# Performance work log

Hardware: AMD Instinct MI355X
Metric: run time of the kernel (lower is better)

The kernel has to match this reference:

```python
import jax, jax.numpy as jnp
import numpy as np

B, S, QD, KVD, H = 8, 1024, 1024, 1024, 8
NEG_SLOPE = 0.01


def _lin(t, w, b):
    # torch nn.Linear: y = x @ W^T + b, W is (out, in)
    return t @ w.T + b


def _heads(t, n_head):
    b, s, e = t.shape
    return t.reshape(b, s, n_head, e // n_head).transpose(0, 2, 1, 3)  # (B,H,S,D)


def _merge(t):
    b, h, s, d = t.shape
    return t.transpose(0, 2, 1, 3).reshape(b, s, h * d)


def setup_inputs() -> dict:
    key = jax.random.key(0)
    ks = iter(jax.random.split(key, 64))

    def W(shape):
        return (jax.random.normal(next(ks), shape, jnp.float32) * 0.02)

    inp = {
        'x': jax.random.normal(next(ks), (B, S, QD), jnp.float32),
        'y': jax.random.normal(next(ks), (B, S, KVD), jnp.float32),
        # cross-attention projections
        'ca_q_w': W((QD, QD)), 'ca_q_b': W((QD,)),
        'ca_qv_w': W((QD, QD)), 'ca_qv_b': W((QD,)),
        'ca_k_w': W((QD, KVD)), 'ca_k_b': W((QD,)),
        'ca_kv_w': W((QD, KVD)), 'ca_kv_b': W((QD,)),
        'ca_o_w': W((QD, QD)), 'ca_o_b': W((QD,)),
        # LayerNorm over [seq_len, q_dim]
        'ln_w': jnp.ones((S, QD), jnp.float32),
        'ln_b': jnp.zeros((S, QD), jnp.float32),
        # 3-layer FeedForward
        'ff1_w': W((QD, QD)), 'ff1_b': W((QD,)),
        'ff2_w': W((QD, QD)), 'ff2_b': W((QD,)),
        'ff3_w': W((QD, QD)), 'ff3_b': W((QD,)),
        # self-attention 1
        'sa1_q_w': W((QD, QD)), 'sa1_q_b': W((QD,)),
        'sa1_k_w': W((QD, QD)), 'sa1_k_b': W((QD,)),
        'sa1_v_w': W((QD, QD)), 'sa1_v_b': W((QD,)),
        'sa1_o_w': W((QD, QD)), 'sa1_o_b': W((QD,)),
        # self-attention 2
        'sa2_q_w': W((QD, QD)), 'sa2_q_b': W((QD,)),
        'sa2_k_w': W((QD, QD)), 'sa2_k_b': W((QD,)),
        'sa2_v_w': W((QD, QD)), 'sa2_v_b': W((QD,)),
        'sa2_o_w': W((QD, QD)), 'sa2_o_b': W((QD,)),
    }
    return inp


def _self_attn(t, qw, qb, kw, kb, vw, vb, ow, ob):
    q = _heads(_lin(t, qw, qb), H)
    k = _heads(_lin(t, kw, kb), H)
    v = _heads(_lin(t, vw, vb), H)
    scale = 1.0 / jnp.sqrt(jnp.asarray(q.shape[-1], q.dtype))
    a = jax.nn.softmax(jnp.einsum('bhsd,bhtd->bhst', q, k) * scale, axis=-1)
    return _lin(_merge(jnp.einsum('bhst,bhtd->bhsd', a, v)), ow, ob)


def reference(x, y, ca_q_w, ca_q_b, ca_qv_w, ca_qv_b, ca_k_w, ca_k_b, ca_kv_w, ca_kv_b, ca_o_w, ca_o_b, ln_w, ln_b, ff1_w, ff1_b, ff2_w, ff2_b, ff3_w, ff3_b, sa1_q_w, sa1_q_b, sa1_k_w, sa1_k_b, sa1_v_w, sa1_v_b, sa1_o_w, sa1_o_b, sa2_q_w, sa2_q_b, sa2_k_w, sa2_k_b, sa2_v_w, sa2_v_b, sa2_o_w, sa2_o_b):
    # --- FlowFace cross-attention (no 1/sqrt(d) scaling, +QV term) ---
    q = _heads(_lin(x, ca_q_w, ca_q_b), H)
    qv = _heads(_lin(x, ca_qv_w, ca_qv_b), H)
    k = _heads(_lin(y, ca_k_w, ca_k_b), H)
    kv = _heads(_lin(y, ca_kv_w, ca_kv_b), H)
    attn = jax.nn.softmax(jnp.einsum('bhsd,bhtd->bhst', q, k), axis=-1)
    ca = _lin(_merge(jnp.einsum('bhst,bhtd->bhsd', attn, kv) + qv), ca_o_w, ca_o_b)
    h1 = x + ca
    # --- LayerNorm over last two dims [seq_len, q_dim] ---
    mu = h1.mean(axis=(-2, -1), keepdims=True)
    var = h1.var(axis=(-2, -1), keepdims=True)
    hn = (h1 - mu) / jnp.sqrt(var + 1e-5) * ln_w + ln_b
    # --- 3-layer FeedForward with leaky_relu + residual ---
    lr = lambda t: jax.nn.leaky_relu(t, NEG_SLOPE)
    f = lr(_lin(lr(_lin(lr(_lin(hn, ff1_w, ff1_b)), ff2_w, ff2_b)), ff3_w, ff3_b))
    h2 = hn + f
    # --- two self-attention layers ---
    h3 = _self_attn(h2, sa1_q_w, sa1_q_b, sa1_k_w, sa1_k_b, sa1_v_w, sa1_v_b, sa1_o_w, sa1_o_b)
    out = _self_attn(h3, sa2_q_w, sa2_q_b, sa2_k_w, sa2_k_b, sa2_v_w, sa2_v_b, sa2_o_w, sa2_o_b)
    return out
```

## Files before the change

kernel.cpp:

```cpp
#include <hip/hip_runtime.h>
#include <cstdint>
#include <cstddef>

#define DI __device__ __forceinline__

typedef __bf16 bf16x8 __attribute__((ext_vector_type(8)));
typedef float  f32x4  __attribute__((ext_vector_type(4)));

constexpr int kE = 1024;
constexpr int kM = 8192;
constexpr float kSlope = 0.01f;

DI float bf2f(ushort u) { union { uint32_t i; float f; } v; v.i = ((uint32_t)u) << 16; return v.f; }
DI ushort f2bf(float f) {
    union { float f; uint32_t i; } v; v.f = f;
    return (ushort)((v.i + 0x7FFFu + ((v.i >> 16) & 1u)) >> 16);
}
DI bf16x8 ld8f(const float* p) {
    const float4 f0 = *(const float4*)p;
    const float4 f1 = *(const float4*)(p + 4);
    union { bf16x8 v; ushort u[8]; } o;
    o.u[0] = f2bf(f0.x); o.u[1] = f2bf(f0.y); o.u[2] = f2bf(f0.z); o.u[3] = f2bf(f0.w);
    o.u[4] = f2bf(f1.x); o.u[5] = f2bf(f1.y); o.u[6] = f2bf(f1.z); o.u[7] = f2bf(f1.w);
    return o.v;
}
template<typename T> DI float ldf(const T* p);
template<> DI float ldf<ushort>(const ushort* p) { return bf2f(*p); }
template<> DI float ldf<float>(const float* p) { return *p; }

DI void gload16(const void* g, void* lds) {
    __builtin_amdgcn_global_load_lds((const __attribute__((address_space(1))) void*)g,
                                     (__attribute__((address_space(3))) void*)lds, 16, 0, 0);
}

DI int swz7(int r) { return ((r ^ (r >> 3)) & 7) << 4; }

struct PtrTab { const float* w[16]; const float* b[16]; const float* x; const float* y; };

__global__ __launch_bounds__(256)
void cvt_pack(PtrTab t, ushort* __restrict__ WB, ushort* __restrict__ Xb,
              ushort* __restrict__ Yb, float* __restrict__ BP)
{
    const int blk = blockIdx.x, tid = threadIdx.x;
    if (blk < 16384) {
        const float* src; ushort* dst; size_t idx;
        if (blk < 8192)       { const int w = blk >> 9; idx = (size_t)(blk & 511) * 2048 + tid * 8; src = t.w[w]; dst = WB + (size_t)w * 1048576; }
        else if (blk < 12288) { idx = (size_t)(blk - 8192) * 2048 + tid * 8;  src = t.x; dst = Xb; }
        else                  { idx = (size_t)(blk - 12288) * 2048 + tid * 8; src = t.y; dst = Yb; }
        *(bf16x8*)(dst + idx) = ld8f(src + idx);
    } else {
        const size_t i = (size_t)(blk - 16384) * 2048 + tid * 8;
        const int w = (int)(i >> 10), off = (int)(i & 1023);
        *(float4*)(BP + i)     = *(const float4*)(t.b[w] + off);
        *(float4*)(BP + i + 4) = *(const float4*)(t.b[w] + off + 4);
    }
}

template<int ACT, int RESID, int VT, typename TR, typename TO>
__global__ __launch_bounds__(256)
void gemm_bf16(const ushort* __restrict__ A, const ushort* __restrict__ W,
               const float* __restrict__ bias, const TR* __restrict__ resb,
               TO* __restrict__ out, int N, ushort* __restrict__ vt_out, int vtcol0)
{
    __shared__ __align__(16) char sm[2][16384];
    constexpr int K = 1024;
    const int tid = threadIdx.x, l = tid & 63, wid = tid >> 6;
    const int wm = wid >> 1, wn = wid & 1;

    const int cpx = gridDim.x >> 3;
    const int sb = (blockIdx.x & 7) * cpx + (blockIdx.x >> 3);
    const int nbn = N >> 7;
    const int bm = sb / nbn, bn = sb - bm * nbn;
    const size_t row0 = (size_t)bm << 7, col0 = (size_t)bn << 7;
    const bool isvt = VT && ((int)col0 >= vtcol0);

    const int o0 = (wid * 2) * 1024 + (l << 4), o1 = o0 + 1024;
    const int r0s = o0 >> 6, c0s = ((o0 >> 4) & 3) ^ ((r0s >> 1) & 3);
    const int r1s = o1 >> 6, c1s = ((o1 >> 4) & 3) ^ ((r1s >> 1) & 3);
    const ushort* gA0 = A + (row0 + r0s) * K + c0s * 8;
    const ushort* gA1 = A + (row0 + r1s) * K + c1s * 8;
    const ushort* gW0 = W + (col0 + r0s) * K + c0s * 8;
    const ushort* gW1 = W + (col0 + r1s) * K + c1s * 8;
    const int d0 = (wid * 2) * 1024, d1 = d0 + 1024;

    f32x4 acc[4][4] = {};

    {
        gload16(gA0, sm[0] + d0); gload16(gA1, sm[0] + d1);
        gload16(gW0, sm[0] + 8192 + d0); gload16(gW1, sm[0] + 8192 + d1);
    }
    __syncthreads();

    for (int kt = 0; kt < 32; ++kt) {
        const int cur = kt & 1;
        if (kt + 1 < 32) {
            const int ko = (kt + 1) << 5;
            char* nb = sm[cur ^ 1];
            gload16(gA0 + ko, nb + d0); gload16(gA1 + ko, nb + d1);
            gload16(gW0 + ko, nb + 8192 + d0); gload16(gW1 + ko, nb + 8192 + d1);
        }
        const char* At = sm[cur];
        const char* Wt = sm[cur] + 8192;
        bf16x8 af[4], bfr[4];
        #pragma unroll
        for (int mi = 0; mi < 4; ++mi) {
            const int r = (wm << 6) + (mi << 4) + (l & 15);
            af[mi] = *(const bf16x8*)(At + r * 64 + ((((l >> 4) ^ ((r >> 1) & 3))) << 4));
        }
        #pragma unroll
        for (int ni = 0; ni < 4; ++ni) {
            const int r = (wn << 6) + (ni << 4) + (l & 15);
            bfr[ni] = *(const bf16x8*)(Wt + r * 64 + ((((l >> 4) ^ ((r >> 1) & 3))) << 4));
        }
        if (!isvt) {
            #pragma unroll
            for (int mi = 0; mi < 4; ++mi)
                #pragma unroll
                for (int ni = 0; ni < 4; ++ni)
                    acc[mi][ni] = __builtin_amdgcn_mfma_f32_16x16x32_bf16(af[mi], bfr[ni], acc[mi][ni], 0, 0, 0);
        } else {
            #pragma unroll
            for (int mi = 0; mi < 4; ++mi)
                #pragma unroll
                for (int ni = 0; ni < 4; ++ni)
                    acc[mi][ni] = __builtin_amdgcn_mfma_f32_16x16x32_bf16(bfr[ni], af[mi], acc[mi][ni], 0, 0, 0);
        }
        __syncthreads();
    }

    const int cr = (l >> 4) << 2, cc = l & 15;
    if (!isvt) {
        #pragma unroll
        for (int mi = 0; mi < 4; ++mi) {
            #pragma unroll
            for (int ni = 0; ni < 4; ++ni) {
                const size_t gr = row0 + (wm << 6) + (mi << 4) + cr;
                const size_t gc = col0 + (wn << 6) + (ni << 4) + cc;
                const float bv = bias[gc];
                #pragma unroll
                for (int r = 0; r < 4; ++r) {
                    float v = acc[mi][ni][r] + bv;
                    if (ACT) v = v > 0.f ? v : v * kSlope;
                    const size_t off = (gr + r) * (size_t)N + gc;
                    if (RESID) v += ldf(resb + off);
                    if constexpr (sizeof(TO) == 4) out[off] = v;
                    else                           out[off] = f2bf(v);
                }
            }
        }
    } else if (VT) {
        #pragma unroll
        for (int mi = 0; mi < 4; ++mi) {
            const size_t t_glob = row0 + (wm << 6) + (mi << 4) + cc;
            const size_t bb = t_glob >> 10;
            const int tt = (int)(t_glob & 1023);
            #pragma unroll
            for (int ni = 0; ni < 4; ++ni) {
                const int gcb = (int)col0 + (wn << 6) + (ni << 4) + cr;
                const int dbase = gcb - vtcol0;
                #pragma unroll
                for (int r = 0; r < 4; ++r) {
                    const float v = acc[mi][ni][r] + bias[gcb + r];
                    vt_out[(((bb << 10) + dbase + r) << 10) + tt] = f2bf(v);
                }
            }
        }
    }
}

template<int ADD_QV>
__global__ __launch_bounds__(256)
void attn_fwd(const ushort* __restrict__ Q, const ushort* __restrict__ K,
              const ushort* __restrict__ VT, const ushort* __restrict__ QV,
              ushort* __restrict__ O, int ld, float scale)
{
    __shared__ __align__(16) char Kt[64 * 256];
    __shared__ __align__(16) char Vt[128 * 128];
    __shared__ __align__(16) char Pl[4][2048];

    const int tid = threadIdx.x;
    const int l = tid & 63, w = tid >> 6;

    const int cpx = gridDim.x >> 3;
    const int sb = (blockIdx.x & 7) * cpx + (blockIdx.x >> 3);
    const int qt = sb & 15;
    const int bh = sb >> 4;
    const int h = bh & 7, b = bh >> 3;

    const size_t bi = ((size_t)b << 10) * (size_t)ld + ((size_t)h << 7);
    const size_t bo = ((size_t)b << 10) * 1024 + ((size_t)h << 7);
    const size_t vtoff = ((size_t)bh) << 17;
    const size_t qrow0 = (size_t)(qt << 6) + (w << 4);

    bf16x8 qf[4];
    #pragma unroll
    for (int kk = 0; kk < 4; ++kk)
        qf[kk] = *(const bf16x8*)(Q + bi + (qrow0 + (l & 15)) * ld + (kk << 5) + ((l >> 4) << 3));

    f32x4 oacc[8] = {};
    float mrow[4] = {-1e30f, -1e30f, -1e30f, -1e30f};
    float lrow[4] = {0.f, 0.f, 0.f, 0.f};

    const int sr = tid >> 4, sc = tid & 15;

    int vofs[4];
    #pragma unroll
    for (int it = 0; it < 4; ++it) {
        const int d = it * 32 + (tid >> 3);
        const int s = tid & 7;
        const int c = s ^ ((d ^ (d >> 3)) & 7);
        vofs[it] = d * 1024 + c * 8;
    }
    const int vdst = tid * 16;

    for (int kt0 = 0; kt0 < 16; ++kt0) {
        __syncthreads();
        #pragma unroll
        for (int it = 0; it < 4; ++it) {
            const int r = sr + (it << 4);
            uint4 kv = *(const uint4*)(K + bi + (size_t)(kt0 * 64 + r) * ld + (sc << 3));
            *(uint4*)(Kt + r * 256 + ((sc << 4) ^ swz7(r))) = kv;
        }
        #pragma unroll
        for (int it = 0; it < 4; ++it) {
            uint4 vv = *(const uint4*)(VT + vtoff + (size_t)(kt0 << 6) + vofs[it]);
            *(uint4*)(Vt + it * 4096 + vdst) = vv;
        }
        __syncthreads();

        f32x4 sacc[4] = {};
        #pragma unroll
        for (int ni = 0; ni < 4; ++ni) {
            const int r = (l & 15) + (ni << 4);
            #pragma unroll
            for (int kk = 0; kk < 4; ++kk) {
                bf16x8 kf = *(const bf16x8*)(Kt + r * 256 + ((((kk << 2) + (l >> 4)) << 4) ^ swz7(r)));
                sacc[ni] = __builtin_amdgcn_mfma_f32_16x16x32_bf16(qf[kk], kf, sacc[ni], 0, 0, 0);
            }
        }
        #pragma unroll
        for (int ni = 0; ni < 4; ++ni) sacc[ni] *= scale;

        float corr[4];
        #pragma unroll
        for (int r = 0; r < 4; ++r) {
            float m0 = fmaxf(fmaxf(sacc[0][r], sacc[1][r]), fmaxf(sacc[2][r], sacc[3][r]));
            #pragma unroll
            for (int m = 1; m < 16; m <<= 1) m0 = fmaxf(m0, __shfl_xor(m0, m, 64));
            const float mn = fmaxf(mrow[r], m0);
            corr[r] = __expf(mrow[r] - mn);
            mrow[r] = mn;
        }
        float ps[4] = {0.f, 0.f, 0.f, 0.f};
        ushort pb[4][4];
        #pragma unroll
        for (int ni = 0; ni < 4; ++ni)
            #pragma unroll
            for (int r = 0; r < 4; ++r) {
                const float p = __expf(sacc[ni][r] - mrow[r]);
                ps[r] += p;
                pb[ni][r] = f2bf(p);
            }
        #pragma unroll
        for (int r = 0; r < 4; ++r) {
            float s = ps[r];
            #pragma unroll
            for (int m = 1; m < 16; m <<= 1) s += __shfl_xor(s, m, 64);
            lrow[r] = lrow[r] * corr[r] + s;
        }
        #pragma unroll
        for (int nd = 0; nd < 8; ++nd)
            #pragma unroll
            for (int r = 0; r < 4; ++r) oacc[nd][r] *= corr[r];

        char* pw = Pl[w];
        #pragma unroll
        for (int ni = 0; ni < 4; ++ni)
            #pragma unroll
            for (int r = 0; r < 4; ++r) {
                const int q = ((l >> 4) << 2) + r;
                const int t = (l & 15) + (ni << 4);
                *(ushort*)(pw + q * 128 + ((t * 2) ^ swz7(q))) = pb[ni][r];
            }
        #pragma unroll
        for (int tg = 0; tg < 2; ++tg) {
            const int q = l & 15;
            bf16x8 pf = *(const bf16x8*)(pw + q * 128 + ((((tg << 2) + (l >> 4)) << 4) ^ swz7(q)));
            #pragma unroll
            for (int nd = 0; nd < 8; ++nd) {
                const int d = (nd << 4) + (l & 15);
                const int m = (d ^ (d >> 3)) & 7;
                bf16x8 vf = *(const bf16x8*)(Vt + d * 128 + ((((tg << 2) + (l >> 4)) ^ m) << 4));
                oacc[nd] = __builtin_amdgcn_mfma_f32_16x16x32_bf16(pf, vf, oacc[nd], 0, 0, 0);
            }
        }
    }

    const size_t orow = qrow0 + ((l >> 4) << 2);
    #pragma unroll
    for (int r = 0; r < 4; ++r) {
        const float inv = 1.f / lrow[r];
        #pragma unroll
        for (int nd = 0; nd < 8; ++nd) {
            const size_t c = (l & 15) + (nd << 4);
            float v = oacc[nd][r] * inv;
            if (ADD_QV) v += bf2f(QV[bi + (orow + r) * ld + c]);
            O[bo + (orow + r) * 1024 + c] = f2bf(v);
        }
    }
}

__global__ void ln_partial(const ushort* __restrict__ h1, float2* __restrict__ part)
{
    __shared__ float sa[8];
    const size_t off = ((size_t)blockIdx.x) << 15;
    float s = 0.f, s2 = 0.f;
    for (int i = threadIdx.x; i < 4096; i += 256) {
        uint4 u = *(const uint4*)(h1 + off + (size_t)i * 8);
        const ushort* e = (const ushort*)&u;
        #pragma unroll
        for (int j = 0; j < 8; ++j) { const float v = bf2f(e[j]); s += v; s2 += v * v; }
    }
    #pragma unroll
    for (int m = 1; m < 64; m <<= 1) { s += __shfl_xor(s, m, 64); s2 += __shfl_xor(s2, m, 64); }
    const int w = threadIdx.x >> 6;
    if ((threadIdx.x & 63) == 0) { sa[w * 2] = s; sa[w * 2 + 1] = s2; }
    __syncthreads();
    if (threadIdx.x == 0)
        part[blockIdx.x] = make_float2(sa[0] + sa[2] + sa[4] + sa[6], sa[1] + sa[3] + sa[5] + sa[7]);
}

__global__ void ln_finish(const float2* __restrict__ part, float2* __restrict__ stats)
{
    const int b = threadIdx.x;
    if (b < 8) {
        float s = 0.f, s2 = 0.f;
        for (int c = 0; c < 32; ++c) { const float2 v = part[b * 32 + c]; s += v.x; s2 += v.y; }
        const float mu = s * (1.f / 1048576.f);
        const float var = s2 * (1.f / 1048576.f) - mu * mu;
        stats[b] = make_float2(mu, rsqrtf(var + 1e-5f));
    }
}

__global__ void ln_apply(const ushort* __restrict__ h1, const float2* __restrict__ stats,
                         const float* __restrict__ gw, const float* __restrict__ gb,
                         ushort* __restrict__ hn)
{
    const size_t i = ((size_t)blockIdx.x * 256 + threadIdx.x) * 8;
    const int b = (int)(i >> 20);
    const size_t r = i & 1048575;
    const float2 st = stats[b];
    uint4 uv = *(const uint4*)(h1 + i);
    const float4 w0 = *(const float4*)(gw + r);
    const float4 w1 = *(const float4*)(gw + r + 4);
    const float4 b0 = *(const float4*)(gb + r);
    const float4 b1 = *(const float4*)(gb + r + 4);
    const float wv[8] = {w0.x, w0.y, w0.z, w0.w, w1.x, w1.y, w1.z, w1.w};
    const float bv[8] = {b0.x, b0.y, b0.z, b0.w, b1.x, b1.y, b1.z, b1.w};
    const ushort* ev = (const ushort*)&uv;
    ushort o[8];
    #pragma unroll
    for (int j = 0; j < 8; ++j)
        o[j] = f2bf((bf2f(ev[j]) - st.x) * st.y * wv[j] + bv[j]);
    *(uint4*)(hn + i) = *(const uint4*)o;
}

extern "C" void kernel_launch(void* const* d_in, const int* in_sizes, int n_in,
                              void* d_out, int out_size, void* d_ws, size_t ws_size,
                              hipStream_t stream)
{
    (void)in_sizes; (void)n_in; (void)out_size; (void)ws_size;
    auto P = [&](int i) { return (const float*)d_in[i]; };

    const size_t MB = 1u << 20;
    char* ws = (char*)d_ws;
    ushort* WB = (ushort*)ws;
    ushort* R0 = (ushort*)(ws + 32 * MB);
    ushort* R1 = (ushort*)(ws + 64 * MB);
    ushort* A0 = (ushort*)(ws + 96 * MB);
    ushort* A1 = (ushort*)(ws + 112 * MB);
    float*  BP = (float*)(ws + 128 * MB);
    float2* PART = (float2*)(ws + 128 * MB + 65536);
    float2* STATS = PART + 256;

    PtrTab tab;
    const int wsrc[16] = {2,4,6,8,10,14,16,18,20,22,24,26,28,30,32,34};
    for (int i = 0; i < 16; ++i) { tab.w[i] = P(wsrc[i]); tab.b[i] = P(wsrc[i] + 1); }
    tab.x = P(0); tab.y = P(1);

    const dim3 blk(256);
    const float SA_SCALE = 0.08838834764831845f;
    auto Wp = [&](int w) { return WB + (size_t)w * 1048576; };
    auto Bp = [&](int w) { return BP + (size_t)w * 1024; };

    cvt_pack<<<dim3(16392), blk, 0, stream>>>(tab, WB, A0, A1, BP);

    gemm_bf16<0,0,0,ushort,ushort><<<dim3(1024), blk, 0, stream>>>(A0, Wp(0), Bp(0), (const ushort*)nullptr, R0, 2048, nullptr, 0);
    gemm_bf16<0,0,1,ushort,ushort><<<dim3(1024), blk, 0, stream>>>(A1, Wp(2), Bp(2), (const ushort*)nullptr, R1, 2048, A0, 1024);
    attn_fwd<1><<<dim3(1024), blk, 0, stream>>>(R0, R1, A0, R0 + 1024, A1, 2048, 1.0f);
    gemm_bf16<0,1,0,float,ushort><<<dim3(512), blk, 0, stream>>>(A1, Wp(4), Bp(4), P(0), A0, 1024, nullptr, 0);

    ln_partial<<<dim3(256), blk, 0, stream>>>(A0, PART);
    ln_finish<<<dim3(1), dim3(64), 0, stream>>>(PART, STATS);
    ln_apply<<<dim3(4096), blk, 0, stream>>>(A0, STATS, P(12), P(13), A1);

    gemm_bf16<1,0,0,ushort,ushort><<<dim3(512), blk, 0, stream>>>(A1, Wp(5), Bp(5), (const ushort*)nullptr, R0, 1024, nullptr, 0);
    gemm_bf16<1,0,0,ushort,ushort><<<dim3(512), blk, 0, stream>>>(R0, Wp(6), Bp(6), (const ushort*)nullptr, R1, 1024, nullptr, 0);
    gemm_bf16<1,1,0,ushort,ushort><<<dim3(512), blk, 0, stream>>>(R1, Wp(7), Bp(7), A1, A0, 1024, nullptr, 0);

    gemm_bf16<0,0,1,ushort,ushort><<<dim3(1536), blk, 0, stream>>>(A0, Wp(8), Bp(8), (const ushort*)nullptr, R0, 3072, A1, 2048);
    attn_fwd<0><<<dim3(1024), blk, 0, stream>>>(R0, R0 + 1024, A1, nullptr, A0, 3072, SA_SCALE);
    gemm_bf16<0,0,0,ushort,ushort><<<dim3(512), blk, 0, stream>>>(A0, Wp(11), Bp(11), (const ushort*)nullptr, A1, 1024, nullptr, 0);

    gemm_bf16<0,0,1,ushort,ushort><<<dim3(1536), blk, 0, stream>>>(A1, Wp(12), Bp(12), (const ushort*)nullptr, R0, 3072, A0, 2048);
    attn_fwd<0><<<dim3(1024), blk, 0, stream>>>(R0, R0 + 1024, A0, nullptr, A1, 3072, SA_SCALE);
    gemm_bf16<0,0,0,ushort,float><<<dim3(512), blk, 0, stream>>>(A1, Wp(15), Bp(15), (const ushort*)nullptr, (float*)d_out, 1024, nullptr, 0);
}
```

Baseline: 876.3 us.

## Add 256x256-tile GEMM kernel for wide fused QKV projections

Adds a new 512-thread GEMM kernel with 256x256 output tiles and 8x4 MFMA accumulators per wave, and uses it for the wide fused projection GEMMs (N=2048/3072), including the transposed-V write path. The 128x128 kernel is kept for the N=1024 GEMMs but loses its VT path. Larger tiles raise arithmetic intensity and cut redundant A/W loads. The cost is more registers and LDS per block and fewer blocks (256/384) to spread across the CUs, which can leave wave slots idle.

```diff
diff --git a/kernel.cpp b/kernel.cpp
--- a/kernel.cpp
+++ b/kernel.cpp
@@ -56,11 +56,11 @@
     }
 }
 
-template<int ACT, int RESID, int VT, typename TR, typename TO>
+template<int ACT, int RESID, typename TR, typename TO>
 __global__ __launch_bounds__(256)
 void gemm_bf16(const ushort* __restrict__ A, const ushort* __restrict__ W,
                const float* __restrict__ bias, const TR* __restrict__ resb,
-               TO* __restrict__ out, int N, ushort* __restrict__ vt_out, int vtcol0)
+               TO* __restrict__ out, int N)
 {
     __shared__ __align__(16) char sm[2][16384];
     constexpr int K = 1024;
@@ -72,7 +72,6 @@
     const int nbn = N >> 7;
     const int bm = sb / nbn, bn = sb - bm * nbn;
     const size_t row0 = (size_t)bm << 7, col0 = (size_t)bn << 7;
-    const bool isvt = VT && ((int)col0 >= vtcol0);
 
     const int o0 = (wid * 2) * 1024 + (l << 4), o1 = o0 + 1024;
     const int r0s = o0 >> 6, c0s = ((o0 >> 4) & 3) ^ ((r0s >> 1) & 3);
@@ -112,15 +111,96 @@
             const int r = (wn << 6) + (ni << 4) + (l & 15);
             bfr[ni] = *(const bf16x8*)(Wt + r * 64 + ((((l >> 4) ^ ((r >> 1) & 3))) << 4));
         }
+        #pragma unroll
+        for (int mi = 0; mi < 4; ++mi)
+            #pragma unroll
+            for (int ni = 0; ni < 4; ++ni)
+                acc[mi][ni] = __builtin_amdgcn_mfma_f32_16x16x32_bf16(af[mi], bfr[ni], acc[mi][ni], 0, 0, 0);
+        __syncthreads();
+    }
+
+    const int cr = (l >> 4) << 2, cc = l & 15;
+    #pragma unroll
+    for (int mi = 0; mi < 4; ++mi) {
+        #pragma unroll
+        for (int ni = 0; ni < 4; ++ni) {
+            const size_t gr = row0 + (wm << 6) + (mi << 4) + cr;
+            const size_t gc = col0 + (wn << 6) + (ni << 4) + cc;
+            const float bv = bias[gc];
+            #pragma unroll
+            for (int r = 0; r < 4; ++r) {
+                float v = acc[mi][ni][r] + bv;
+                if (ACT) v = v > 0.f ? v : v * kSlope;
+                const size_t off = (gr + r) * (size_t)N + gc;
+                if (RESID) v += ldf(resb + off);
+                if constexpr (sizeof(TO) == 4) out[off] = v;
+                else                           out[off] = f2bf(v);
+            }
+        }
+    }
+}
+
+template<int VT>
+__global__ __launch_bounds__(512, 2)
+void gemm256(const ushort* __restrict__ A, const ushort* __restrict__ W,
+             const float* __restrict__ bias, ushort* __restrict__ out, int N,
+             ushort* __restrict__ vt_out, int vtcol0)
+{
+    __shared__ __align__(16) char sm[2][32768];
+    constexpr int K = 1024;
+    const int tid = threadIdx.x, l = tid & 63, wid = tid >> 6;
+    const int wm = wid >> 2, wn = wid & 3;
+
+    const int cpx = gridDim.x >> 3;
+    const int sb = (blockIdx.x & 7) * cpx + (blockIdx.x >> 3);
+    const int nbn = N >> 8;
+    const int bm = sb / nbn, bn = sb - bm * nbn;
+    const size_t row0 = (size_t)bm << 8, col0 = (size_t)bn << 8;
+    const bool isvt = VT && ((int)col0 >= vtcol0);
+
+    const int r0s = tid >> 2, c0s = (tid & 3) ^ ((r0s >> 1) & 3);
+    const ushort* gA0 = A + (row0 + r0s) * K + c0s * 8;
+    const ushort* gA1 = gA0 + (size_t)128 * K;
+    const ushort* gW0 = W + (col0 + r0s) * K + c0s * 8;
+    const ushort* gW1 = gW0 + (size_t)128 * K;
+    const int d0 = wid * 1024;
+
+    f32x4 acc[8][4] = {};
+
+    gload16(gA0, sm[0] + d0);          gload16(gA1, sm[0] + 8192 + d0);
+    gload16(gW0, sm[0] + 16384 + d0);  gload16(gW1, sm[0] + 24576 + d0);
+    __syncthreads();
+
+    for (int kt = 0; kt < 32; ++kt) {
+        const int cur = kt & 1;
+        if (kt + 1 < 32) {
+            const int ko = (kt + 1) << 5;
+            char* nb = sm[cur ^ 1];
+            gload16(gA0 + ko, nb + d0);          gload16(gA1 + ko, nb + 8192 + d0);
+            gload16(gW0 + ko, nb + 16384 + d0);  gload16(gW1 + ko, nb + 24576 + d0);
+        }
+        const char* At = sm[cur];
+        const char* Wt = sm[cur] + 16384;
+        bf16x8 af[8], bfr[4];
+        #pragma unroll
+        for (int mi = 0; mi < 8; ++mi) {
+            const int r = (wm << 7) + (mi << 4) + (l & 15);
+            af[mi] = *(const bf16x8*)(At + r * 64 + (((l >> 4) ^ ((r >> 1) & 3)) << 4));
+        }
+        #pragma unroll
+        for (int ni = 0; ni < 4; ++ni) {
+            const int r = (wn << 6) + (ni << 4) + (l & 15);
+            bfr[ni] = *(const bf16x8*)(Wt + r * 64 + (((l >> 4) ^ ((r >> 1) & 3)) << 4));
+        }
         if (!isvt) {
             #pragma unroll
-            for (int mi = 0; mi < 4; ++mi)
+            for (int mi = 0; mi < 8; ++mi)
                 #pragma unroll
                 for (int ni = 0; ni < 4; ++ni)
                     acc[mi][ni] = __builtin_amdgcn_mfma_f32_16x16x32_bf16(af[mi], bfr[ni], acc[mi][ni], 0, 0, 0);
         } else {
             #pragma unroll
-            for (int mi = 0; mi < 4; ++mi)
+            for (int mi = 0; mi < 8; ++mi)
                 #pragma unroll
                 for (int ni = 0; ni < 4; ++ni)
                     acc[mi][ni] = __builtin_amdgcn_mfma_f32_16x16x32_bf16(bfr[ni], af[mi], acc[mi][ni], 0, 0, 0);
@@ -131,27 +211,23 @@
     const int cr = (l >> 4) << 2, cc = l & 15;
     if (!isvt) {
         #pragma unroll
-        for (int mi = 0; mi < 4; ++mi) {
+        for (int mi = 0; mi < 8; ++mi) {
             #pragma unroll
             for (int ni = 0; ni < 4; ++ni) {
-                const size_t gr = row0 + (wm << 6) + (mi << 4) + cr;
+                const size_t gr = row0 + (wm << 7) + (mi << 4) + cr;
                 const size_t gc = col0 + (wn << 6) + (ni << 4) + cc;
                 const float bv = bias[gc];
                 #pragma unroll
                 for (int r = 0; r < 4; ++r) {
-                    float v = acc[mi][ni][r] + bv;
-                    if (ACT) v = v > 0.f ? v : v * kSlope;
-                    const size_t off = (gr + r) * (size_t)N + gc;
-                    if (RESID) v += ldf(resb + off);
-                    if constexpr (sizeof(TO) == 4) out[off] = v;
-                    else                           out[off] = f2bf(v);
+                    const float v = acc[mi][ni][r] + bv;
+                    out[(gr + r) * (size_t)N + gc] = f2bf(v);
                 }
             }
         }
     } else if (VT) {
         #pragma unroll
-        for (int mi = 0; mi < 4; ++mi) {
-            const size_t t_glob = row0 + (wm << 6) + (mi << 4) + cc;
+        for (int mi = 0; mi < 8; ++mi) {
+            const size_t t_glob = row0 + (wm << 7) + (mi << 4) + cc;
             const size_t bb = t_glob >> 10;
             const int tt = (int)(t_glob & 1023);
             #pragma unroll
@@ -388,31 +464,31 @@
     for (int i = 0; i < 16; ++i) { tab.w[i] = P(wsrc[i]); tab.b[i] = P(wsrc[i] + 1); }
     tab.x = P(0); tab.y = P(1);
 
-    const dim3 blk(256);
+    const dim3 blk(256), blk5(512);
     const float SA_SCALE = 0.08838834764831845f;
     auto Wp = [&](int w) { return WB + (size_t)w * 1048576; };
     auto Bp = [&](int w) { return BP + (size_t)w * 1024; };
 
     cvt_pack<<<dim3(16392), blk, 0, stream>>>(tab, WB, A0, A1, BP);
 
-    gemm_bf16<0,0,0,ushort,ushort><<<dim3(1024), blk, 0, stream>>>(A0, Wp(0), Bp(0), (const ushort*)nullptr, R0, 2048, nullptr, 0);
-    gemm_bf16<0,0,1,ushort,ushort><<<dim3(1024), blk, 0, stream>>>(A1, Wp(2), Bp(2), (const ushort*)nullptr, R1, 2048, A0, 1024);
+    gemm256<0><<<dim3(256), blk5, 0, stream>>>(A0, Wp(0), Bp(0), R0, 2048, nullptr, 0);
+    gemm256<1><<<dim3(256), blk5, 0, stream>>>(A1, Wp(2), Bp(2), R1, 2048, A0, 1024);
     attn_fwd<1><<<dim3(1024), blk, 0, stream>>>(R0, R1, A0, R0 + 1024, A1, 2048, 1.0f);
-    gemm_bf16<0,1,0,float,ushort><<<dim3(512), blk, 0, stream>>>(A1, Wp(4), Bp(4), P(0), A0, 1024, nullptr, 0);
+    gemm_bf16<0,1,float,ushort><<<dim3(512), blk, 0, stream>>>(A1, Wp(4), Bp(4), P(0), A0, 1024);
 
     ln_partial<<<dim3(256), blk, 0, stream>>>(A0, PART);
     ln_finish<<<dim3(1), dim3(64), 0, stream>>>(PART, STATS);
     ln_apply<<<dim3(4096), blk, 0, stream>>>(A0, STATS, P(12), P(13), A1);
 
-    gemm_bf16<1,0,0,ushort,ushort><<<dim3(512), blk, 0, stream>>>(A1, Wp(5), Bp(5), (const ushort*)nullptr, R0, 1024, nullptr, 0);
-    gemm_bf16<1,0,0,ushort,ushort><<<dim3(512), blk, 0, stream>>>(R0, Wp(6), Bp(6), (const ushort*)nullptr, R1, 1024, nullptr, 0);
-    gemm_bf16<1,1,0,ushort,ushort><<<dim3(512), blk, 0, stream>>>(R1, Wp(7), Bp(7), A1, A0, 1024, nullptr, 0);
-
-    gemm_bf16<0,0,1,ushort,ushort><<<dim3(1536), blk, 0, stream>>>(A0, Wp(8), Bp(8), (const ushort*)nullptr, R0, 3072, A1, 2048);
+    gemm_bf16<1,0,ushort,ushort><<<dim3(512), blk, 0, stream>>>(A1, Wp(5), Bp(5), (const ushort*)nullptr, R0, 1024);
+    gemm_bf16<1,0,ushort,ushort><<<dim3(512), blk, 0, stream>>>(R0, Wp(6), Bp(6), (const ushort*)nullptr, R1, 1024);
+    gemm_bf16<1,1,ushort,ushort><<<dim3(512), blk, 0, stream>>>(R1, Wp(7), Bp(7), A1, A0, 1024);
+
+    gemm256<1><<<dim3(384), blk5, 0, stream>>>(A0, Wp(8), Bp(8), R0, 3072, A1, 2048);
     attn_fwd<0><<<dim3(1024), blk, 0, stream>>>(R0, R0 + 1024, A1, nullptr, A0, 3072, SA_SCALE);
-    gemm_bf16<0,0,0,ushort,ushort><<<dim3(512), blk, 0, stream>>>(A0, Wp(11), Bp(11), (const ushort*)nullptr, A1, 1024, nullptr, 0);
-
-    gemm_bf16<0,0,1,ushort,ushort><<<dim3(1536), blk, 0, stream>>>(A1, Wp(12), Bp(12), (const ushort*)nullptr, R0, 3072, A0, 2048);
+    gemm_bf16<0,0,ushort,ushort><<<dim3(512), blk, 0, stream>>>(A0, Wp(11), Bp(11), (const ushort*)nullptr, A1, 1024);
+
+    gemm256<1><<<dim3(384), blk5, 0, stream>>>(A1, Wp(12), Bp(12), R0, 3072, A0, 2048);
     attn_fwd<0><<<dim3(1024), blk, 0, stream>>>(R0, R0 + 1024, A0, nullptr, A1, 3072, SA_SCALE);
-    gemm_bf16<0,0,0,ushort,float><<<dim3(512), blk, 0, stream>>>(A1, Wp(15), Bp(15), (const ushort*)nullptr, (float*)d_out, 1024, nullptr, 0);
-}
+    gemm_bf16<0,0,ushort,float><<<dim3(512), blk, 0, stream>>>(A1, Wp(15), Bp(15), (const ushort*)nullptr, (float*)d_out, 1024);
+}
```

After: 1.669 ms. +90.5%, slower.
